# Optimization experiments

Hardware: AMD Instinct MI355X
Metric: run time of the kernel (lower is better)

## Reference

```python
import jax, jax.numpy as jnp
import numpy as np
from functools import partial

B, S, D_IN, H = 8, 2048, 1024, 1024
V = 50257
NUM_CODEWORDS, EMB_DIM = 256, 16
NUM_NEURONS, TOP_K = 64, 16  # top_k = sparsity(0.25) * 64
TILE_ROWS = 16
NUM_TILES = H // TILE_ROWS  # 64 -> decoder out_features = 1024
FREQS = (1.0, 2.0, 4.0)
MAX_LEN = 1024


def setup_inputs() -> dict:
    key = jax.random.key(0)
    ks = jax.random.split(key, 16)
    s = 0.02
    return {
        "inputs": jax.random.normal(ks[0], (B, S, D_IN), jnp.float32),
        "Wt": jax.random.normal(ks[1], (H, D_IN), jnp.float32) * s,
        "bt": jnp.zeros((H,), jnp.float32),
        "Wq": jax.random.normal(ks[2], (H, H), jnp.float32) * s,
        "bq": jnp.zeros((H,), jnp.float32),
        "Wk": jax.random.normal(ks[3], (H, H), jnp.float32) * s,
        "bk": jnp.zeros((H,), jnp.float32),
        "Wv": jax.random.normal(ks[4], (H, H), jnp.float32) * s,
        "bv": jnp.zeros((H,), jnp.float32),
        "Wo": jax.random.normal(ks[5], (D_IN, H), jnp.float32) * s,
        "bo": jnp.zeros((D_IN,), jnp.float32),
        "codebook": jax.random.normal(ks[6], (NUM_CODEWORDS, EMB_DIM), jnp.float32) * s,
        "instructions": jax.random.randint(ks[7], (NUM_TILES * TILE_ROWS, D_IN // EMB_DIM), 0, NUM_CODEWORDS),
        "W_lm": jax.random.normal(ks[8], (V, NUM_TILES * TILE_ROWS), jnp.float32) * s,
        "b_lm": jnp.zeros((V,), jnp.float32),
    }


def _positional_bias(seq_len):
    # AttentionBasisSynthesizer: sin/cos atoms at freqs (1,2,4), gains=1, shifts=0
    ang = 2.0 * jnp.pi * jnp.arange(seq_len, dtype=jnp.float32) / MAX_LEN
    bias = jnp.zeros((seq_len,), jnp.float32)
    for f in FREQS:
        bias = bias + jnp.sin(f * ang) + jnp.cos(f * ang)
    return bias  # [S]


def _forward(inputs, Wt, bt, Wq, bq, Wk, bk, Wv, bv, Wo, bo, codebook, instructions, W_lm, b_lm):
    tokens = inputs @ Wt.T + bt                       # [B,S,H]
    q = tokens @ Wq.T + bq
    k = tokens @ Wk.T + bk
    v = tokens @ Wv.T + bv
    # per-step KV-cache loop == causal attention over prefix; vectorize
    scores = jnp.einsum("bqh,bkh->bqk", q, k) / jnp.sqrt(jnp.float32(H))
    scores = scores + _positional_bias(S)[None, None, :]
    i = jnp.arange(S)
    causal = i[:, None] >= i[None, :]                 # [S,S]
    scores = jnp.where(causal[None], scores, -jnp.inf)
    attn = jnp.einsum("bqk,bkh->bqh", jax.nn.softmax(scores, axis=-1), v)  # [B,S,H]
    # sparse routing: group into NUM_NEURONS neurons, keep top-k by L2 norm,
    # softmax weights over kept neurons, straight-through combine with dense path
    g = attn.reshape(B, S, NUM_NEURONS, H // NUM_NEURONS)
    sc = jnp.sqrt(jnp.sum(g * g, axis=-1))            # [B,S,N]
    vals, idx = jax.lax.top_k(sc, TOP_K)              # [B,S,K]
    w = jax.nn.softmax(vals, axis=-1)
    onehot = jax.nn.one_hot(idx, NUM_NEURONS, dtype=attn.dtype)  # [B,S,K,N]
    wfull = jnp.einsum("bsk,bskn->bsn", w, onehot)    # [B,S,N]
    combined = (g * wfull[..., None]).reshape(B, S, H)
    combined = combined + (attn - jax.lax.stop_gradient(attn))  # straight-through
    dec_in = combined @ Wo.T + bo                     # [B,S,D_IN]
    x = jnp.mean(dec_in, axis=1)                      # [B,D_IN]
    # DemopackDecoder: weight rows assembled from codebook via instruction indices
    W_dec = codebook[instructions].reshape(NUM_TILES * TILE_ROWS, D_IN)
    hidden = x @ W_dec.T                              # [B, 1024]
    return hidden @ W_lm.T + b_lm                     # [B, V]


def reference(inputs, Wt, bt, Wq, bq, Wk, bk, Wv, bv, Wo, bo, codebook, instructions, W_lm, b_lm):
    return _forward(inputs, Wt, bt, Wq, bq, Wk, bk, Wv, bv, Wo, bo, codebook, instructions, W_lm, b_lm)
```

## Files before the change

kernel.cpp:

```cpp
#include <hip/hip_runtime.h>
#include <cstdint>
#include <cstddef>

#define B_   8
#define S_   2048
#define DIN_ 1024
#define H_   1024
#define V_   50257

typedef unsigned short ushort_t;
typedef __bf16 bf16x8 __attribute__((ext_vector_type(8)));
typedef float  f32x4  __attribute__((ext_vector_type(4)));

__device__ __forceinline__ ushort_t f2bf(float x) {
    unsigned u = __float_as_uint(x);
    u = (u + 0x7fffu + ((u >> 16) & 1u)) >> 16;
    return (ushort_t)u;
}

__device__ __forceinline__ void async16(const void* g, void* s) {
    __builtin_amdgcn_global_load_lds(
        (const __attribute__((address_space(1))) unsigned int*)g,
        (__attribute__((address_space(3))) unsigned int*)s, 16, 0, 0);
}

__device__ __forceinline__ float wredmax(float v) {
#pragma unroll
    for (int o = 32; o; o >>= 1) v = fmaxf(v, __shfl_xor(v, o));
    return v;
}
__device__ __forceinline__ float wredsum(float v) {
#pragma unroll
    for (int o = 32; o; o >>= 1) v += __shfl_xor(v, o);
    return v;
}

__global__ void f2bf_vec(const float* __restrict__ in, ushort_t* __restrict__ out, int n4) {
    int i = blockIdx.x * 256 + threadIdx.x;
    if (i >= n4) return;
    float4 f = ((const float4*)in)[i];
    ushort4 u;
    u.x = f2bf(f.x); u.y = f2bf(f.y); u.z = f2bf(f.z); u.w = f2bf(f.w);
    ((ushort4*)out)[i] = u;
}

__global__ void pos_bias_kernel(float* __restrict__ bias) {
    int k = blockIdx.x * 256 + threadIdx.x;
    if (k >= S_) return;
    float ang = 6.283185307179586f * (float)k / 1024.0f;
    float b = 0.f;
    b += sinf(1.f * ang) + cosf(1.f * ang);
    b += sinf(2.f * ang) + cosf(2.f * ang);
    b += sinf(4.f * ang) + cosf(4.f * ang);
    bias[k] = b;
}

__global__ __launch_bounds__(256)
void transpose_wt(const float* __restrict__ Wt, ushort_t* __restrict__ wtT) {
    __shared__ float t[64][65];
    int k0 = blockIdx.x * 64, i0 = blockIdx.y * 64;
    int tx = threadIdx.x & 63, ty = threadIdx.x >> 6;
#pragma unroll
    for (int j = 0; j < 16; j++) {
        int k = ty * 16 + j;
        t[k][tx] = Wt[(size_t)(k0 + k) * DIN_ + i0 + tx];
    }
    __syncthreads();
#pragma unroll
    for (int j = 0; j < 16; j++) {
        int i = ty * 16 + j;
        wtT[(size_t)(i0 + i) * H_ + k0 + tx] = f2bf(t[tx][i]);
    }
}

__global__ __launch_bounds__(256)
void bcomb_kernel(const float* __restrict__ Wq, const float* __restrict__ Wk,
                  const float* __restrict__ Wv, const float* __restrict__ bq,
                  const float* __restrict__ bk, const float* __restrict__ bv,
                  const float* __restrict__ bt, float* __restrict__ bcomb) {
    int wave = threadIdx.x >> 6, lane = threadIdx.x & 63;
    int j = blockIdx.x * 4 + wave;
    const float* W  = j < 1024 ? Wq : (j < 2048 ? Wk : Wv);
    const float* bb = j < 1024 ? bq : (j < 2048 ? bk : bv);
    int rowj = j & 1023;
    const float4* wr4 = (const float4*)(W + (size_t)rowj * 1024);
    const float4* bt4 = (const float4*)bt;
    float s = 0.f;
#pragma unroll
    for (int c = 0; c < 4; c++) {
        float4 w = wr4[c * 64 + lane];
        float4 b = bt4[c * 64 + lane];
        s += w.x * b.x + w.y * b.y + w.z * b.z + w.w * b.w;
    }
    s = wredsum(s);
    if (lane == 0) bcomb[j] = s + bb[rowj];
}

template <int OUT_BF16>
__global__ __launch_bounds__(256)
void gemm_bt(const ushort_t* __restrict__ A, int lda,
             const ushort_t* __restrict__ Bt, int ldb,
             void* __restrict__ Cv, int ldc, int K, const float* __restrict__ bias) {
    int bn = blockIdx.x, bm = blockIdx.y;
    __shared__ ushort_t As[128 * 32];
    __shared__ ushort_t Bs[128 * 32];
    int tid = threadIdx.x, wave = tid >> 6, lane = tid & 63;
    int wr = wave >> 1, wc = wave & 1;
    int nkt = K >> 5;
    int srow = lane >> 2, scol = (lane & 3) * 8;
    size_t arow0 = (size_t)bm * 128, brow0 = (size_t)bn * 128;
    f32x4 acc[4][4];
#pragma unroll
    for (int m = 0; m < 4; m++)
#pragma unroll
        for (int n = 0; n < 4; n++) acc[m][n] = f32x4{0.f, 0.f, 0.f, 0.f};
    for (int kt = 0; kt < nkt; ++kt) {
        int k0 = kt * 32;
#pragma unroll
        for (int i = 0; i < 2; i++) {
            int reg = wave * 2 + i;
            int row = reg * 16 + srow;
            async16(A + (arow0 + row) * (size_t)lda + k0 + scol, (ushort_t*)As + reg * 512);
            async16(Bt + (brow0 + row) * (size_t)ldb + k0 + scol, (ushort_t*)Bs + reg * 512);
        }
        __syncthreads();
        bf16x8 af[4], bfr[4];
#pragma unroll
        for (int m = 0; m < 4; m++)
            af[m] = *(const bf16x8*)&As[(wr * 64 + m * 16 + (lane & 15)) * 32 + (lane >> 4) * 8];
#pragma unroll
        for (int n = 0; n < 4; n++)
            bfr[n] = *(const bf16x8*)&Bs[(wc * 64 + n * 16 + (lane & 15)) * 32 + (lane >> 4) * 8];
#pragma unroll
        for (int m = 0; m < 4; m++)
#pragma unroll
            for (int n = 0; n < 4; n++)
                acc[m][n] = __builtin_amdgcn_mfma_f32_16x16x32_bf16(af[m], bfr[n], acc[m][n], 0, 0, 0);
        __syncthreads();
    }
    int rl = (lane >> 4) * 4, cl = lane & 15;
#pragma unroll
    for (int m = 0; m < 4; m++)
#pragma unroll
        for (int n = 0; n < 4; n++) {
            int col = bn * 128 + wc * 64 + n * 16 + cl;
            float badd = bias ? bias[col] : 0.f;
#pragma unroll
            for (int r = 0; r < 4; r++) {
                int row = bm * 128 + wr * 64 + m * 16 + rl + r;
                float v = acc[m][n][r] + badd;
                size_t off = (size_t)row * ldc + col;
                if (OUT_BF16) ((ushort_t*)Cv)[off] = f2bf(v);
                else          ((float*)Cv)[off] = v;
            }
        }
}

template <int OUT_BF16, int CAUSAL_SKIP, int KLIM>
__global__ __launch_bounds__(512, 2)
void gemm256(const ushort_t* __restrict__ A, size_t sAb, int lda,
             const ushort_t* __restrict__ Bt, size_t sBb, int ldb,
             void* __restrict__ Cv, size_t sCb, int ldc,
             int K, const float* __restrict__ bias, int nbn, int nwg) {
    int orig = blockIdx.x, bz = blockIdx.y;
    int qq = nwg >> 3, rr8 = nwg & 7;
    int xcd = orig & 7, idx = orig >> 3;
    int wgid = (xcd < rr8 ? xcd * (qq + 1) : rr8 * (qq + 1) + (xcd - rr8) * qq) + idx;
    int bm = wgid / nbn, bn = wgid - bm * nbn;
    if (CAUSAL_SKIP && bn > bm) return;

    __shared__ float4 lds4[6144];
    char* lds = (char*)lds4;

    const ushort_t* Ab = A + (size_t)bz * sAb;
    const ushort_t* Bb = Bt + (size_t)bz * sBb;

    int tid = threadIdx.x, wave = tid >> 6, lane = tid & 63;
    int wr = wave >> 2, wc = wave & 3;

    int kmax = K;
    if (KLIM) { int km = (bm + 1) * 256; kmax = km < K ? km : K; }
    int nkt = kmax >> 5;

    size_t arow0 = (size_t)bm * 256, brow0 = (size_t)bn * 256;

    int gswz = ((tid & 3) ^ ((tid >> 3) & 3)) * 8;
    const ushort_t* Ag = Ab + (arow0 + (tid >> 2)) * (size_t)lda + gswz;
    const ushort_t* Bg = Bb + (brow0 + (tid >> 2)) * (size_t)ldb + gswz;
    int stg_wbase = wave * 1024;

    int fr = lane & 15;
    int kb_sw = (((lane >> 4) ^ ((lane >> 1) & 3)) << 4);
    int a_off = (wr * 128 + fr) * 64 + kb_sw;
    int b_off = 16384 + (wc * 64 + fr) * 64 + kb_sw;

    f32x4 acc[8][4];
#pragma unroll
    for (int m = 0; m < 8; m++)
#pragma unroll
        for (int n = 0; n < 4; n++) acc[m][n] = f32x4{0.f, 0.f, 0.f, 0.f};

#define STAGE_A(t, sb)                                                         \
    do {                                                                       \
        const ushort_t* g_ = Ag + (size_t)(t) * 32;                            \
        char* d_ = lds + (sb) * 32768 + stg_wbase;                             \
        async16(g_, d_);                                                       \
        async16(g_ + (size_t)128 * lda, d_ + 8192);                            \
    } while (0)
#define STAGE_B(t, sb)                                                         \
    do {                                                                       \
        const ushort_t* g_ = Bg + (size_t)(t) * 32;                            \
        char* d_ = lds + (sb) * 32768 + 16384 + stg_wbase;                     \
        async16(g_, d_);                                                       \
        async16(g_ + (size_t)128 * ldb, d_ + 8192);                            \
    } while (0)

    STAGE_A(0, 0); STAGE_B(0, 0);
    STAGE_A(1, 1); STAGE_B(1, 1);
    asm volatile("s_waitcnt vmcnt(4)" ::: "memory");
    __builtin_amdgcn_s_barrier();

    int cur = 0;
    for (int t = 0; t < nkt; ++t) {
        char* base = lds + cur * 32768;
        int stg = cur == 0 ? 2 : cur - 1;
        bool do_stage = (t + 2) < nkt;

        bf16x8 af[8], b0, b1;
#pragma unroll
        for (int mf = 0; mf < 8; mf++)
            af[mf] = *(const bf16x8*)(base + a_off + mf * 1024);
        b0 = *(const bf16x8*)(base + b_off);
        b1 = *(const bf16x8*)(base + b_off + 1024);
        if (do_stage) STAGE_A(t + 2, stg);
        __builtin_amdgcn_s_barrier();
        asm volatile("s_waitcnt lgkmcnt(0)" ::: "memory");
        __builtin_amdgcn_sched_barrier(0);
        __builtin_amdgcn_s_setprio(1);
#pragma unroll
        for (int mf = 0; mf < 8; mf++) {
            acc[mf][0] = __builtin_amdgcn_mfma_f32_16x16x32_bf16(af[mf], b0, acc[mf][0], 0, 0, 0);
            acc[mf][1] = __builtin_amdgcn_mfma_f32_16x16x32_bf16(af[mf], b1, acc[mf][1], 0, 0, 0);
        }
        __builtin_amdgcn_s_setprio(0);
        __builtin_amdgcn_s_barrier();

        bf16x8 b2, b3;
        b2 = *(const bf16x8*)(base + b_off + 2048);
        b3 = *(const bf16x8*)(base + b_off + 3072);
        if (do_stage) STAGE_B(t + 2, stg);
        __builtin_amdgcn_s_barrier();
        asm volatile("s_waitcnt lgkmcnt(0)" ::: "memory");
        __builtin_amdgcn_sched_barrier(0);
        __builtin_amdgcn_s_setprio(1);
#pragma unroll
        for (int mf = 0; mf < 8; mf++) {
            acc[mf][2] = __builtin_amdgcn_mfma_f32_16x16x32_bf16(af[mf], b2, acc[mf][2], 0, 0, 0);
            acc[mf][3] = __builtin_amdgcn_mfma_f32_16x16x32_bf16(af[mf], b3, acc[mf][3], 0, 0, 0);
        }
        __builtin_amdgcn_s_setprio(0);
        if (do_stage)         asm volatile("s_waitcnt vmcnt(4)" ::: "memory");
        else if (t + 1 < nkt) asm volatile("s_waitcnt vmcnt(0)" ::: "memory");
        __builtin_amdgcn_s_barrier();

        cur = cur == 2 ? 0 : cur + 1;
    }
#undef STAGE_A
#undef STAGE_B

    int rl = (lane >> 4) * 4, cl = lane & 15;
#pragma unroll
    for (int mf = 0; mf < 8; mf++)
#pragma unroll
        for (int nf = 0; nf < 4; nf++) {
            int col = bn * 256 + wc * 64 + nf * 16 + cl;
            float badd = bias ? bias[col] : 0.f;
#pragma unroll
            for (int r = 0; r < 4; r++) {
                int row = bm * 256 + wr * 128 + mf * 16 + rl + r;
                float v = acc[mf][nf][r] + badd;
                size_t off = (size_t)bz * sCb + (size_t)row * ldc + col;
                if (OUT_BF16) ((ushort_t*)Cv)[off] = f2bf(v);
                else          ((float*)Cv)[off] = v;
            }
        }
}

__global__ __launch_bounds__(256)
void transpose_v(const ushort_t* __restrict__ qkv, ushort_t* __restrict__ vT) {
    __shared__ ushort_t t[64][66];
    int b = blockIdx.z;
    int s0 = blockIdx.x * 64, h0 = blockIdx.y * 64;
    int tx = threadIdx.x & 63, ty = threadIdx.x >> 6;
#pragma unroll
    for (int i = 0; i < 16; i++) {
        int s = ty * 16 + i;
        t[s][tx] = qkv[((size_t)b * S_ + s0 + s) * 3072 + 2048 + h0 + tx];
    }
    __syncthreads();
#pragma unroll
    for (int i = 0; i < 16; i++) {
        int h = ty * 16 + i;
        vT[((size_t)b * H_ + h0 + h) * S_ + s0 + tx] = t[tx][h];
    }
}

__global__ __launch_bounds__(256)
void softmax_kernel(const float* __restrict__ scores, ushort_t* __restrict__ P,
                    const float* __restrict__ bias) {
    __shared__ float srs[S_];
    __shared__ float red[8];
    int q = blockIdx.x, b = blockIdx.y;
    int L = q + 1;
    int tid = threadIdx.x;
    const float* srow = scores + ((size_t)b * S_ + q) * S_;
    const float scale = 0.03125f;

    float lm = -3e38f;
    for (int k = tid; k < L; k += 256) {
        float s = srow[k] * scale + bias[k];
        srs[k] = s;
        lm = fmaxf(lm, s);
    }
    lm = wredmax(lm);
    if ((tid & 63) == 0) red[tid >> 6] = lm;
    __syncthreads();
    float m = fmaxf(fmaxf(red[0], red[1]), fmaxf(red[2], red[3]));

    float ls = 0.f;
    for (int k = tid; k < L; k += 256) {
        float e = __expf(srs[k] - m);
        srs[k] = e;
        ls += e;
    }
    ls = wredsum(ls);
    if ((tid & 63) == 0) red[4 + (tid >> 6)] = ls;
    __syncthreads();
    float invs = 1.f / (red[4] + red[5] + red[6] + red[7]);

    int kz = ((q >> 8) + 1) * 256;
    ushort_t* prow = P + ((size_t)b * S_ + q) * S_;
    for (int k = tid; k < kz; k += 256)
        prow[k] = (k < L) ? f2bf(srs[k] * invs) : (ushort_t)0;
}

__global__ __launch_bounds__(256)
void routing_kernel(const float* __restrict__ attn, ushort_t* __restrict__ combined) {
    int wave = threadIdx.x >> 6, lane = threadIdx.x & 63;
    size_t row = (size_t)blockIdx.x * 4 + wave;
    const float4* a4 = (const float4*)(attn + row * H_);
    float4 x0 = a4[lane * 4 + 0], x1 = a4[lane * 4 + 1];
    float4 x2 = a4[lane * 4 + 2], x3 = a4[lane * 4 + 3];
    float ss = x0.x * x0.x + x0.y * x0.y + x0.z * x0.z + x0.w * x0.w
             + x1.x * x1.x + x1.y * x1.y + x1.z * x1.z + x1.w * x1.w
             + x2.x * x2.x + x2.y * x2.y + x2.z * x2.z + x2.w * x2.w
             + x3.x * x3.x + x3.y * x3.y + x3.z * x3.z + x3.w * x3.w;
    float sc = sqrtf(ss);

    float v = sc, thr = 0.f, mx = 0.f;
#pragma unroll
    for (int i = 0; i < 16; i++) {
        float mm = wredmax(v);
        if (i == 0) mx = mm;
        thr = mm;
        if (v == mm) v = -1e30f;
    }
    float e = (sc >= thr) ? __expf(sc - mx) : 0.f;
    float se = wredsum(e);
    float w = e / se;

    const float xs[16] = {x0.x, x0.y, x0.z, x0.w, x1.x, x1.y, x1.z, x1.w,
                          x2.x, x2.y, x2.z, x2.w, x3.x, x3.y, x3.z, x3.w};
    union { ushort_t u[16]; uint4 q[2]; } pk;
#pragma unroll
    for (int j = 0; j < 16; j++) pk.u[j] = f2bf(xs[j] * w);
    uint4* dst = (uint4*)(combined + row * H_ + lane * 16);
    dst[0] = pk.q[0];
    dst[1] = pk.q[1];
}

__global__ void cmean_part(const ushort_t* __restrict__ comb, float* __restrict__ part) {
    int d = blockIdx.x * 256 + threadIdx.x;
    int sc = blockIdx.y, b = blockIdx.z;
    const ushort_t* p = comb + ((size_t)b * S_ + sc * 128) * H_ + d;
    float s = 0.f;
    for (int i = 0; i < 128; i++) s += __uint_as_float((unsigned)p[(size_t)i * H_] << 16);
    part[((size_t)b * 16 + sc) * H_ + d] = s;
}

__global__ void cmean_final(const float* __restrict__ part, float* __restrict__ cm) {
    int idx = blockIdx.x * 256 + threadIdx.x;
    int b = idx >> 10, d = idx & 1023;
    float s = 0.f;
#pragma unroll
    for (int c = 0; c < 16; c++) s += part[((size_t)b * 16 + c) * DIN_ + d];
    cm[idx] = s * (1.0f / 2048.0f);
}

__global__ __launch_bounds__(256)
void xgemv(const float* __restrict__ cm, const float* __restrict__ Wo,
           const float* __restrict__ bo, float* __restrict__ x) {
    int wave = threadIdx.x >> 6, lane = threadIdx.x & 63;
    int i = blockIdx.x * 4 + wave;
    const float4* wr4 = (const float4*)(Wo + (size_t)i * H_);
    float4 w[4];
#pragma unroll
    for (int c = 0; c < 4; c++) w[c] = wr4[c * 64 + lane];
    float accv[B_];
#pragma unroll
    for (int b = 0; b < B_; b++) {
        const float4* c4 = (const float4*)(cm + (size_t)b * H_);
        float s = 0.f;
#pragma unroll
        for (int c = 0; c < 4; c++) {
            float4 h = c4[c * 64 + lane];
            s += w[c].x * h.x + w[c].y * h.y + w[c].z * h.z + w[c].w * h.w;
        }
        accv[b] = wredsum(s);
    }
    if (lane == 0) {
        float bi = bo[i];
#pragma unroll
        for (int b = 0; b < B_; b++) x[(size_t)b * DIN_ + i] = accv[b] + bi;
    }
}

__global__ __launch_bounds__(64)
void decode_hidden(const float* __restrict__ x, const float* __restrict__ codebook,
                   const int* __restrict__ instr, float* __restrict__ hidden) {
    int r = blockIdx.x;
    int lane = threadIdx.x;
    int idx = instr[r * 64 + lane];
    const float4* cw = (const float4*)(codebook + (size_t)idx * 16);
    float4 c0 = cw[0], c1 = cw[1], c2 = cw[2], c3 = cw[3];
    float acc[B_];
#pragma unroll
    for (int b = 0; b < B_; b++) {
        const float4* xb = (const float4*)(x + (size_t)b * DIN_ + lane * 16);
        float4 h0 = xb[0], h1 = xb[1], h2 = xb[2], h3 = xb[3];
        acc[b] = c0.x * h0.x + c0.y * h0.y + c0.z * h0.z + c0.w * h0.w
               + c1.x * h1.x + c1.y * h1.y + c1.z * h1.z + c1.w * h1.w
               + c2.x * h2.x + c2.y * h2.y + c2.z * h2.z + c2.w * h2.w
               + c3.x * h3.x + c3.y * h3.y + c3.z * h3.z + c3.w * h3.w;
    }
#pragma unroll
    for (int b = 0; b < B_; b++) acc[b] = wredsum(acc[b]);
    if (lane == 0) {
#pragma unroll
        for (int b = 0; b < B_; b++) hidden[(size_t)b * 1024 + r] = acc[b];
    }
}

__global__ __launch_bounds__(256)
void lm_head(const float* __restrict__ Wlm, const float* __restrict__ hidden,
             const float* __restrict__ blm, float* __restrict__ out) {
    int wave = threadIdx.x >> 6, lane = threadIdx.x & 63;
    for (int v = blockIdx.x * 4 + wave; v < V_; v += gridDim.x * 4) {
        const float4* wrow = (const float4*)(Wlm + (size_t)v * 1024);
        float acc[B_];
#pragma unroll
        for (int b = 0; b < B_; b++) acc[b] = 0.f;
#pragma unroll
        for (int rr = 0; rr < 4; rr++) {
            float4 wv = wrow[rr * 64 + lane];
#pragma unroll
            for (int b = 0; b < B_; b++) {
                float4 hv = ((const float4*)hidden)[b * 256 + rr * 64 + lane];
                acc[b] += wv.x * hv.x + wv.y * hv.y + wv.z * hv.z + wv.w * hv.w;
            }
        }
#pragma unroll
        for (int b = 0; b < B_; b++) acc[b] = wredsum(acc[b]);
        if (lane == 0) {
            float bl = blm[v];
#pragma unroll
            for (int b = 0; b < B_; b++) out[(size_t)b * V_ + v] = acc[b] + bl;
        }
    }
}

extern "C" void kernel_launch(void* const* d_in, const int* in_sizes, int n_in,
                              void* d_out, int out_size, void* d_ws, size_t ws_size,
                              hipStream_t stream) {
    const float* inputs = (const float*)d_in[0];
    const float* Wt  = (const float*)d_in[1];
    const float* bt  = (const float*)d_in[2];
    const float* Wq  = (const float*)d_in[3];
    const float* bq  = (const float*)d_in[4];
    const float* Wk  = (const float*)d_in[5];
    const float* bk  = (const float*)d_in[6];
    const float* Wv  = (const float*)d_in[7];
    const float* bv  = (const float*)d_in[8];
    const float* Wo  = (const float*)d_in[9];
    const float* bo  = (const float*)d_in[10];
    const float* codebook = (const float*)d_in[11];
    const int*   instructions = (const int*)d_in[12];
    const float* Wlm = (const float*)d_in[13];
    const float* blm = (const float*)d_in[14];
    float* out = (float*)d_out;

    const size_t MB = 1024 * 1024;
    char* ws = (char*)d_ws;
    ushort_t* wqkv_bf = (ushort_t*)(ws + 0);
    ushort_t* wtT_bf  = (ushort_t*)(ws + 6 * MB);
    ushort_t* wcomb   = (ushort_t*)(ws + 8 * MB);
    float* bcomb  = (float*)(ws + 14 * MB);
    float* pbias  = (float*)(ws + 14 * MB + 64 * 1024);
    float* cm     = (float*)(ws + 14 * MB + 128 * 1024);
    float* xbuf   = (float*)(ws + 14 * MB + 192 * 1024);
    float* hidden = (float*)(ws + 14 * MB + 256 * 1024);
    float* part   = (float*)(ws + 14 * MB + 512 * 1024);
    ushort_t* inbf   = (ushort_t*)(ws + 16 * MB);
    ushort_t* qkv    = (ushort_t*)(ws + 48 * MB);
    ushort_t* vT     = (ushort_t*)(ws + 144 * MB);
    float* scores    = (float*)(ws + 176 * MB);
    ushort_t* P      = (ushort_t*)(ws + 304 * MB);
    float* attn      = (float*)(ws + 48 * MB);
    ushort_t* combined = (ushort_t*)(ws + 176 * MB);

    f2bf_vec<<<16384, 256, 0, stream>>>(inputs, inbf, 4194304);
    f2bf_vec<<<1024, 256, 0, stream>>>(Wq, wqkv_bf, 262144);
    f2bf_vec<<<1024, 256, 0, stream>>>(Wk, wqkv_bf + 1048576, 262144);
    f2bf_vec<<<1024, 256, 0, stream>>>(Wv, wqkv_bf + 2097152, 262144);
    transpose_wt<<<dim3(16, 16), 256, 0, stream>>>(Wt, wtT_bf);
    bcomb_kernel<<<768, 256, 0, stream>>>(Wq, Wk, Wv, bq, bk, bv, bt, bcomb);
    pos_bias_kernel<<<8, 256, 0, stream>>>(pbias);

    gemm_bt<1><<<dim3(8, 24), 256, 0, stream>>>(wqkv_bf, 1024, wtT_bf, 1024,
                                                wcomb, 1024, 1024, nullptr);

    gemm256<1, 0, 0><<<dim3(768, 1), 512, 0, stream>>>(
        inbf, 0, 1024, wcomb, 0, 1024, qkv, 0, 3072, 1024, bcomb, 12, 768);

    transpose_v<<<dim3(32, 16, 8), 256, 0, stream>>>(qkv, vT);

    gemm256<0, 1, 0><<<dim3(64, 8), 512, 0, stream>>>(
        qkv, (size_t)S_ * 3072, 3072, qkv + 1024, (size_t)S_ * 3072, 3072,
        scores, (size_t)S_ * S_, S_, 1024, nullptr, 8, 64);

    softmax_kernel<<<dim3(S_, B_), 256, 0, stream>>>(scores, P, pbias);

    gemm256<0, 0, 1><<<dim3(32, 8), 512, 0, stream>>>(
        P, (size_t)S_ * S_, S_, vT, (size_t)H_ * S_, S_,
        attn, (size_t)S_ * H_, H_, S_, nullptr, 4, 32);

    routing_kernel<<<4096, 256, 0, stream>>>(attn, combined);

    cmean_part<<<dim3(4, 16, 8), 256, 0, stream>>>(combined, part);
    cmean_final<<<32, 256, 0, stream>>>(part, cm);
    xgemv<<<256, 256, 0, stream>>>(cm, Wo, bo, xbuf);

    decode_hidden<<<1024, 64, 0, stream>>>(xbuf, codebook, instructions, hidden);

    lm_head<<<2048, 256, 0, stream>>>(Wlm, hidden, blm, out);
}
```

Before: 481.3 us.

## Restructure gemm256 to BK=64 double-buffered pipeline with register prefetch

Rewrites the main 256x256 GEMM mainloop to take K tiles of 64 instead of 32. It uses two 64KB LDS buffers in dynamic shared memory instead of three 32KB ones, with a new swizzle. Fragments are prefetched in registers across four MFMA quadrants, and global-to-LDS staging is interleaved between them, to halve the per-K-step barrier count and hide LDS latency. It also merges the three Wq/Wk/Wv bf16 conversion launches into one kernel. The 128KB of LDS per block limits occupancy to one 512-thread block per CU, down from two.

```diff
diff --git a/kernel.cpp b/kernel.cpp
--- a/kernel.cpp
+++ b/kernel.cpp
@@ -42,6 +42,17 @@
     ushort4 u;
     u.x = f2bf(f.x); u.y = f2bf(f.y); u.z = f2bf(f.z); u.w = f2bf(f.w);
     ((ushort4*)out)[i] = u;
+}
+
+__global__ void f2bf_w3(const float* __restrict__ Wq, const float* __restrict__ Wk,
+                        const float* __restrict__ Wv, ushort_t* __restrict__ out) {
+    int i = blockIdx.x * 256 + threadIdx.x;
+    int w = i >> 18, off = i & 262143;
+    const float* src = w == 0 ? Wq : (w == 1 ? Wk : Wv);
+    float4 f = ((const float4*)src)[off];
+    ushort4 u;
+    u.x = f2bf(f.x); u.y = f2bf(f.y); u.z = f2bf(f.z); u.w = f2bf(f.w);
+    ((ushort4*)(out + (size_t)w * 1048576))[off] = u;
 }
 
 __global__ void pos_bias_kernel(float* __restrict__ bias) {
@@ -162,37 +173,35 @@
              const ushort_t* __restrict__ Bt, size_t sBb, int ldb,
              void* __restrict__ Cv, size_t sCb, int ldc,
              int K, const float* __restrict__ bias, int nbn, int nwg) {
+    extern __shared__ char lds[];
     int orig = blockIdx.x, bz = blockIdx.y;
     int qq = nwg >> 3, rr8 = nwg & 7;
-    int xcd = orig & 7, idx = orig >> 3;
-    int wgid = (xcd < rr8 ? xcd * (qq + 1) : rr8 * (qq + 1) + (xcd - rr8) * qq) + idx;
+    int xcd = orig & 7, bidx = orig >> 3;
+    int wgid = (xcd < rr8 ? xcd * (qq + 1) : rr8 * (qq + 1) + (xcd - rr8) * qq) + bidx;
     int bm = wgid / nbn, bn = wgid - bm * nbn;
     if (CAUSAL_SKIP && bn > bm) return;
 
-    __shared__ float4 lds4[6144];
-    char* lds = (char*)lds4;
-
     const ushort_t* Ab = A + (size_t)bz * sAb;
     const ushort_t* Bb = Bt + (size_t)bz * sBb;
-
     int tid = threadIdx.x, wave = tid >> 6, lane = tid & 63;
     int wr = wave >> 2, wc = wave & 3;
 
     int kmax = K;
     if (KLIM) { int km = (bm + 1) * 256; kmax = km < K ? km : K; }
-    int nkt = kmax >> 5;
-
-    size_t arow0 = (size_t)bm * 256, brow0 = (size_t)bn * 256;
-
-    int gswz = ((tid & 3) ^ ((tid >> 3) & 3)) * 8;
-    const ushort_t* Ag = Ab + (arow0 + (tid >> 2)) * (size_t)lda + gswz;
-    const ushort_t* Bg = Bb + (brow0 + (tid >> 2)) * (size_t)ldb + gswz;
-    int stg_wbase = wave * 1024;
-
-    int fr = lane & 15;
-    int kb_sw = (((lane >> 4) ^ ((lane >> 1) & 3)) << 4);
-    int a_off = (wr * 128 + fr) * 64 + kb_sw;
-    int b_off = 16384 + (wc * 64 + fr) * 64 + kb_sw;
+    int nkt = kmax >> 6;
+
+    int srow = wave * 8 + (lane >> 3);
+    int sswz = ((lane & 7) ^ (lane >> 3)) * 8;
+    const ushort_t* Ag = Ab + ((size_t)bm * 256 + srow) * (size_t)lda + sswz;
+    const ushort_t* Bg = Bb + ((size_t)bn * 256 + srow) * (size_t)ldb + sswz;
+    int sdst = wave * 1024;
+
+    int fr = lane & 15, g = lane >> 4;
+    int kx = (fr >> 2) & 1;
+    int gsw = (g ^ (fr & 3)) * 16;
+    int aoff = wr * 16384 + fr * 128 + gsw;
+    int boff = 32768 + (wc >> 1) * 16384 + ((wc & 1) * 64 + fr) * 128 + gsw;
+    int ks0 = kx << 6, ks1 = (kx ^ 1) << 6;
 
     f32x4 acc[8][4];
 #pragma unroll
@@ -200,73 +209,125 @@
 #pragma unroll
         for (int n = 0; n < 4; n++) acc[m][n] = f32x4{0.f, 0.f, 0.f, 0.f};
 
-#define STAGE_A(t, sb)                                                         \
+#define STG_A(t, h, bo)                                                        \
     do {                                                                       \
-        const ushort_t* g_ = Ag + (size_t)(t) * 32;                            \
-        char* d_ = lds + (sb) * 32768 + stg_wbase;                             \
-        async16(g_, d_);                                                       \
-        async16(g_ + (size_t)128 * lda, d_ + 8192);                            \
+        async16(Ag + (size_t)((h) * 128) * lda + (t) * 64,                     \
+                lds + (bo) + (h) * 16384 + sdst);                              \
+        async16(Ag + (size_t)((h) * 128 + 64) * lda + (t) * 64,                \
+                lds + (bo) + (h) * 16384 + 8192 + sdst);                       \
     } while (0)
-#define STAGE_B(t, sb)                                                         \
+#define STG_B(t, h, bo)                                                        \
     do {                                                                       \
-        const ushort_t* g_ = Bg + (size_t)(t) * 32;                            \
-        char* d_ = lds + (sb) * 32768 + 16384 + stg_wbase;                     \
-        async16(g_, d_);                                                       \
-        async16(g_ + (size_t)128 * ldb, d_ + 8192);                            \
+        async16(Bg + (size_t)((h) * 128) * ldb + (t) * 64,                     \
+                lds + (bo) + 32768 + (h) * 16384 + sdst);                      \
+        async16(Bg + (size_t)((h) * 128 + 64) * ldb + (t) * 64,                \
+                lds + (bo) + 32768 + (h) * 16384 + 8192 + sdst);               \
     } while (0)
 
-    STAGE_A(0, 0); STAGE_B(0, 0);
-    STAGE_A(1, 1); STAGE_B(1, 1);
-    asm volatile("s_waitcnt vmcnt(4)" ::: "memory");
+    STG_A(0, 0, 0); STG_A(0, 1, 0); STG_B(0, 0, 0); STG_B(0, 1, 0);
+    STG_A(1, 0, 65536); STG_A(1, 1, 65536); STG_B(1, 0, 65536); STG_B(1, 1, 65536);
+    asm volatile("s_waitcnt vmcnt(8)" ::: "memory");
+    __builtin_amdgcn_sched_barrier(0);
     __builtin_amdgcn_s_barrier();
-
-    int cur = 0;
-    for (int t = 0; t < nkt; ++t) {
-        char* base = lds + cur * 32768;
-        int stg = cur == 0 ? 2 : cur - 1;
-        bool do_stage = (t + 2) < nkt;
-
-        bf16x8 af[8], b0, b1;
-#pragma unroll
-        for (int mf = 0; mf < 8; mf++)
-            af[mf] = *(const bf16x8*)(base + a_off + mf * 1024);
-        b0 = *(const bf16x8*)(base + b_off);
-        b1 = *(const bf16x8*)(base + b_off + 1024);
-        if (do_stage) STAGE_A(t + 2, stg);
+    __builtin_amdgcn_sched_barrier(0);
+
+    bf16x8 af03[4][2], af47[4][2], bf01[2][2], bf23[2][2];
+#pragma unroll
+    for (int mf = 0; mf < 4; mf++) {
+        af03[mf][0] = *(const bf16x8*)(lds + aoff + mf * 2048 + ks0);
+        af03[mf][1] = *(const bf16x8*)(lds + aoff + mf * 2048 + ks1);
+    }
+#pragma unroll
+    for (int nf = 0; nf < 2; nf++) {
+        bf01[nf][0] = *(const bf16x8*)(lds + boff + nf * 2048 + ks0);
+        bf01[nf][1] = *(const bf16x8*)(lds + boff + nf * 2048 + ks1);
+    }
+
+    int bufo = 0;
+    for (int t = 0; t < nkt; ++t, bufo ^= 65536) {
+        int nb = bufo ^ 65536;
+#pragma unroll
+        for (int mf = 0; mf < 4; mf++) {
+            af47[mf][0] = *(const bf16x8*)(lds + bufo + aoff + (mf + 4) * 2048 + ks0);
+            af47[mf][1] = *(const bf16x8*)(lds + bufo + aoff + (mf + 4) * 2048 + ks1);
+        }
+#pragma unroll
+        for (int nf = 0; nf < 2; nf++) {
+            bf23[nf][0] = *(const bf16x8*)(lds + bufo + boff + (nf + 2) * 2048 + ks0);
+            bf23[nf][1] = *(const bf16x8*)(lds + bufo + boff + (nf + 2) * 2048 + ks1);
+        }
+        __builtin_amdgcn_s_setprio(1);
+#pragma unroll
+        for (int mf = 0; mf < 4; mf++)
+#pragma unroll
+            for (int nf = 0; nf < 2; nf++) {
+                acc[mf][nf] = __builtin_amdgcn_mfma_f32_16x16x32_bf16(af03[mf][0], bf01[nf][0], acc[mf][nf], 0, 0, 0);
+                acc[mf][nf] = __builtin_amdgcn_mfma_f32_16x16x32_bf16(af03[mf][1], bf01[nf][1], acc[mf][nf], 0, 0, 0);
+            }
+        __builtin_amdgcn_s_setprio(0);
+        __builtin_amdgcn_sched_barrier(0);
         __builtin_amdgcn_s_barrier();
-        asm volatile("s_waitcnt lgkmcnt(0)" ::: "memory");
-        __builtin_amdgcn_sched_barrier(0);
+        __builtin_amdgcn_sched_barrier(0);
+
         __builtin_amdgcn_s_setprio(1);
 #pragma unroll
-        for (int mf = 0; mf < 8; mf++) {
-            acc[mf][0] = __builtin_amdgcn_mfma_f32_16x16x32_bf16(af[mf], b0, acc[mf][0], 0, 0, 0);
-            acc[mf][1] = __builtin_amdgcn_mfma_f32_16x16x32_bf16(af[mf], b1, acc[mf][1], 0, 0, 0);
-        }
+        for (int mf = 0; mf < 4; mf++)
+#pragma unroll
+            for (int nf = 0; nf < 2; nf++) {
+                acc[mf + 4][nf] = __builtin_amdgcn_mfma_f32_16x16x32_bf16(af47[mf][0], bf01[nf][0], acc[mf + 4][nf], 0, 0, 0);
+                acc[mf + 4][nf] = __builtin_amdgcn_mfma_f32_16x16x32_bf16(af47[mf][1], bf01[nf][1], acc[mf + 4][nf], 0, 0, 0);
+            }
         __builtin_amdgcn_s_setprio(0);
+        __builtin_amdgcn_sched_barrier(0);
         __builtin_amdgcn_s_barrier();
-
-        bf16x8 b2, b3;
-        b2 = *(const bf16x8*)(base + b_off + 2048);
-        b3 = *(const bf16x8*)(base + b_off + 3072);
-        if (do_stage) STAGE_B(t + 2, stg);
+        __builtin_amdgcn_sched_barrier(0);
+
+        if (t + 2 < nkt) STG_A(t + 2, 0, bufo);
+        __builtin_amdgcn_s_setprio(1);
+#pragma unroll
+        for (int mf = 0; mf < 4; mf++)
+#pragma unroll
+            for (int nf = 0; nf < 2; nf++) {
+                acc[mf][nf + 2] = __builtin_amdgcn_mfma_f32_16x16x32_bf16(af03[mf][0], bf23[nf][0], acc[mf][nf + 2], 0, 0, 0);
+                acc[mf][nf + 2] = __builtin_amdgcn_mfma_f32_16x16x32_bf16(af03[mf][1], bf23[nf][1], acc[mf][nf + 2], 0, 0, 0);
+            }
+        __builtin_amdgcn_s_setprio(0);
+        __builtin_amdgcn_sched_barrier(0);
+        if (t + 1 < nkt) {
+            if (t + 2 < nkt) { asm volatile("s_waitcnt vmcnt(2)" ::: "memory"); }
+            else             { asm volatile("s_waitcnt vmcnt(0)" ::: "memory"); }
+        }
         __builtin_amdgcn_s_barrier();
-        asm volatile("s_waitcnt lgkmcnt(0)" ::: "memory");
-        __builtin_amdgcn_sched_barrier(0);
+        __builtin_amdgcn_sched_barrier(0);
+
+        if (t + 1 < nkt) {
+#pragma unroll
+            for (int mf = 0; mf < 4; mf++) {
+                af03[mf][0] = *(const bf16x8*)(lds + nb + aoff + mf * 2048 + ks0);
+                af03[mf][1] = *(const bf16x8*)(lds + nb + aoff + mf * 2048 + ks1);
+            }
+#pragma unroll
+            for (int nf = 0; nf < 2; nf++) {
+                bf01[nf][0] = *(const bf16x8*)(lds + nb + boff + nf * 2048 + ks0);
+                bf01[nf][1] = *(const bf16x8*)(lds + nb + boff + nf * 2048 + ks1);
+            }
+        }
+        if (t + 2 < nkt) { STG_A(t + 2, 1, bufo); STG_B(t + 2, 0, bufo); STG_B(t + 2, 1, bufo); }
         __builtin_amdgcn_s_setprio(1);
 #pragma unroll
-        for (int mf = 0; mf < 8; mf++) {
-            acc[mf][2] = __builtin_amdgcn_mfma_f32_16x16x32_bf16(af[mf], b2, acc[mf][2], 0, 0, 0);
-            acc[mf][3] = __builtin_amdgcn_mfma_f32_16x16x32_bf16(af[mf], b3, acc[mf][3], 0, 0, 0);
-        }
+        for (int mf = 0; mf < 4; mf++)
+#pragma unroll
+            for (int nf = 0; nf < 2; nf++) {
+                acc[mf + 4][nf + 2] = __builtin_amdgcn_mfma_f32_16x16x32_bf16(af47[mf][0], bf23[nf][0], acc[mf + 4][nf + 2], 0, 0, 0);
+                acc[mf + 4][nf + 2] = __builtin_amdgcn_mfma_f32_16x16x32_bf16(af47[mf][1], bf23[nf][1], acc[mf + 4][nf + 2], 0, 0, 0);
+            }
         __builtin_amdgcn_s_setprio(0);
-        if (do_stage)         asm volatile("s_waitcnt vmcnt(4)" ::: "memory");
-        else if (t + 1 < nkt) asm volatile("s_waitcnt vmcnt(0)" ::: "memory");
+        __builtin_amdgcn_sched_barrier(0);
         __builtin_amdgcn_s_barrier();
-
-        cur = cur == 2 ? 0 : cur + 1;
-    }
-#undef STAGE_A
-#undef STAGE_B
+        __builtin_amdgcn_sched_barrier(0);
+    }
+#undef STG_A
+#undef STG_B
 
     int rl = (lane >> 4) * 4, cl = lane & 15;
 #pragma unroll
@@ -499,6 +560,13 @@
     const float* blm = (const float*)d_in[14];
     float* out = (float*)d_out;
 
+    (void)hipFuncSetAttribute(reinterpret_cast<const void*>(&gemm256<1, 0, 0>),
+                              hipFuncAttributeMaxDynamicSharedMemorySize, 131072);
+    (void)hipFuncSetAttribute(reinterpret_cast<const void*>(&gemm256<0, 1, 0>),
+                              hipFuncAttributeMaxDynamicSharedMemorySize, 131072);
+    (void)hipFuncSetAttribute(reinterpret_cast<const void*>(&gemm256<0, 0, 1>),
+                              hipFuncAttributeMaxDynamicSharedMemorySize, 131072);
+
     const size_t MB = 1024 * 1024;
     char* ws = (char*)d_ws;
     ushort_t* wqkv_bf = (ushort_t*)(ws + 0);
@@ -519,9 +587,7 @@
     ushort_t* combined = (ushort_t*)(ws + 176 * MB);
 
     f2bf_vec<<<16384, 256, 0, stream>>>(inputs, inbf, 4194304);
-    f2bf_vec<<<1024, 256, 0, stream>>>(Wq, wqkv_bf, 262144);
-    f2bf_vec<<<1024, 256, 0, stream>>>(Wk, wqkv_bf + 1048576, 262144);
-    f2bf_vec<<<1024, 256, 0, stream>>>(Wv, wqkv_bf + 2097152, 262144);
+    f2bf_w3<<<3072, 256, 0, stream>>>(Wq, Wk, Wv, wqkv_bf);
     transpose_wt<<<dim3(16, 16), 256, 0, stream>>>(Wt, wtT_bf);
     bcomb_kernel<<<768, 256, 0, stream>>>(Wq, Wk, Wv, bq, bk, bv, bt, bcomb);
     pos_bias_kernel<<<8, 256, 0, stream>>>(pbias);
@@ -529,18 +595,18 @@
     gemm_bt<1><<<dim3(8, 24), 256, 0, stream>>>(wqkv_bf, 1024, wtT_bf, 1024,
                                                 wcomb, 1024, 1024, nullptr);
 
-    gemm256<1, 0, 0><<<dim3(768, 1), 512, 0, stream>>>(
+    gemm256<1, 0, 0><<<dim3(768, 1), 512, 131072, stream>>>(
         inbf, 0, 1024, wcomb, 0, 1024, qkv, 0, 3072, 1024, bcomb, 12, 768);
 
     transpose_v<<<dim3(32, 16, 8), 256, 0, stream>>>(qkv, vT);
 
-    gemm256<0, 1, 0><<<dim3(64, 8), 512, 0, stream>>>(
+    gemm256<0, 1, 0><<<dim3(64, 8), 512, 131072, stream>>>(
         qkv, (size_t)S_ * 3072, 3072, qkv + 1024, (size_t)S_ * 3072, 3072,
         scores, (size_t)S_ * S_, S_, 1024, nullptr, 8, 64);
 
     softmax_kernel<<<dim3(S_, B_), 256, 0, stream>>>(scores, P, pbias);
 
-    gemm256<0, 0, 1><<<dim3(32, 8), 512, 0, stream>>>(
+    gemm256<0, 0, 1><<<dim3(32, 8), 512, 131072, stream>>>(
         P, (size_t)S_ * S_, S_, vT, (size_t)H_ * S_, S_,
         attn, (size_t)S_ * H_, H_, S_, nullptr, 4, 32);
 
```

New measurement: 459.8 us. 1.05x faster.
